# Kernel optimization log

Hardware: AMD Instinct MI355X
Metric: run time of the kernel (lower is better)

## Reference

```python
import jax, jax.numpy as jnp
import numpy as np

N_EMBD = 1024
N_HEAD = 16
HEAD_DIM = N_EMBD // N_HEAD


def setup_inputs() -> dict:
    key = jax.random.key(0)
    kx, kq, kk, kv, ko = jax.random.split(key, 5)
    B, T = 4, 2048
    x = jax.random.normal(kx, (B, T, N_EMBD), dtype=jnp.float32)
    s = N_EMBD ** -0.5
    Wq = jax.random.normal(kq, (N_EMBD, N_EMBD), dtype=jnp.float32) * s
    Wk = jax.random.normal(kk, (N_EMBD, HEAD_DIM), dtype=jnp.float32) * s
    Wv = jax.random.normal(kv, (N_EMBD, HEAD_DIM), dtype=jnp.float32) * s
    Wo = jax.random.normal(ko, (N_EMBD, N_EMBD), dtype=jnp.float32) * s
    return {"x": x, "Wq": Wq, "Wk": Wk, "Wv": Wv, "Wo": Wo}


def reference(x, Wq, Wk, Wv, Wo):
    B, T, C = x.shape
    scale = HEAD_DIM ** -0.5
    # q: [B, H, T, D]; shared k, v: [B, T, D]
    q = (x @ Wq).reshape(B, T, N_HEAD, HEAD_DIM).transpose(0, 2, 1, 3)
    k = x @ Wk
    v = x @ Wv
    # scores: [B, H, T, T] (shared K head broadcast over H)
    att = jnp.einsum('bhtd,bsd->bhts', q, k) * scale
    causal = jnp.tril(jnp.ones((T, T), dtype=bool))
    att = jnp.where(causal, att, -jnp.inf)
    att = jax.nn.softmax(att, axis=-1)
    out = jnp.einsum('bhts,bsd->bhtd', att, v)  # [B, H, T, D]
    out = out.transpose(0, 2, 1, 3).reshape(B, T, C)
    return out @ Wo
```

## Files before the change

### kernel.cpp

```cpp
#include <hip/hip_runtime.h>

typedef __attribute__((ext_vector_type(8))) short short8;
typedef __attribute__((ext_vector_type(4))) float f32x4;

__device__ __forceinline__ unsigned short f2bf(float f) {
  unsigned u = __builtin_bit_cast(unsigned, f);
  u += 0x7fffu + ((u >> 16) & 1u);
  return (unsigned short)(u >> 16);
}
__device__ __forceinline__ unsigned pack_bf2_rtz(float p0, float p1) {
  return __builtin_amdgcn_perm(__builtin_bit_cast(unsigned, p1),
                               __builtin_bit_cast(unsigned, p0), 0x07060302u);
}

#define GLDS16(g, l)                                                          \
  __builtin_amdgcn_global_load_lds(                                           \
      (const __attribute__((address_space(1))) void*)(g),                     \
      (__attribute__((address_space(3))) void*)(l), 16, 0, 0)

#define QSCALE 0.18033688011112042f

__global__ void cast_x_bf16(const float4* __restrict__ in,
                            ushort4* __restrict__ out, int n4) {
  int i = blockIdx.x * blockDim.x + threadIdx.x;
  if (i >= n4) return;
  float4 v = in[i];
  ushort4 o;
  o.x = f2bf(v.x); o.y = f2bf(v.y); o.z = f2bf(v.z); o.w = f2bf(v.w);
  out[i] = o;
}

__global__ void transpose_cvt_all(const float* __restrict__ Wq,
                                  const float* __restrict__ Wk,
                                  const float* __restrict__ Wv,
                                  const float* __restrict__ Wo,
                                  unsigned short* __restrict__ Wcat,
                                  unsigned short* __restrict__ Wot) {
  __shared__ float tile[32][33];
  const int z = blockIdx.z;
  int bx = blockIdx.x;
  const float* in;
  unsigned short* out;
  int N;
  if (z == 0)      { in = Wq; out = Wcat;               N = 1024; }
  else if (z == 1) { in = Wo; out = Wot;                N = 1024; }
  else {
    if (bx < 2)      { in = Wk; out = Wcat + 1024 * 1024; N = 64; }
    else if (bx < 4) { in = Wv; out = Wcat + 1088 * 1024; N = 64; bx -= 2; }
    else return;
  }
  const int K = 1024;
  const int n0 = bx * 32, k0 = blockIdx.y * 32;
  const int tx = threadIdx.x, ty = threadIdx.y;
#pragma unroll
  for (int i = 0; i < 4; ++i)
    tile[ty + 8 * i][tx] = in[(size_t)(k0 + ty + 8 * i) * N + n0 + tx];
  __syncthreads();
#pragma unroll
  for (int i = 0; i < 4; ++i)
    out[(size_t)(n0 + ty + 8 * i) * K + k0 + tx] = f2bf(tile[tx][ty + 8 * i]);
}

__global__ void transpose_v(const unsigned short* __restrict__ Vr,
                            unsigned short* __restrict__ Vt) {
  __shared__ unsigned short tile[32][34];
  const int t0 = blockIdx.x * 32;
  const int d0 = blockIdx.y * 32;
  const int b = blockIdx.z;
  const int tx = threadIdx.x, ty = threadIdx.y;
#pragma unroll
  for (int i = 0; i < 4; ++i)
    tile[ty + 8 * i][tx] =
        Vr[(size_t)(b * 2048 + t0 + ty + 8 * i) * 64 + d0 + tx];
  __syncthreads();
#pragma unroll
  for (int i = 0; i < 4; ++i)
    Vt[((size_t)b * 64 + d0 + ty + 8 * i) * 2048 + t0 + tx] =
        tile[tx][ty + 8 * i];
}

template <int EPI>
__global__ __launch_bounds__(256) void gemm_bt(
    const unsigned short* __restrict__ A, const unsigned short* __restrict__ Bt,
    unsigned short* __restrict__ Cq, unsigned short* __restrict__ Ck,
    unsigned short* __restrict__ Cv, float* __restrict__ Cf, int N, int K) {
  __shared__ __align__(16) unsigned short As[128 * 64];
  __shared__ __align__(16) unsigned short Bs[128 * 64];
  const int tid = threadIdx.x;
  const int w = tid >> 6, lane = tid & 63;
  const int nwg = gridDim.x * gridDim.y;
  const int lid = blockIdx.y * gridDim.x + blockIdx.x;
  const int cpx = nwg >> 3;
  const int swz = (lid & 7) * cpx + (lid >> 3);
  const int m0 = (swz / gridDim.x) * 128, n0 = (swz % gridDim.x) * 128;
  const int wm = (w >> 1) * 64, wn = (w & 1) * 64;
  const int g = lane >> 4, c = lane & 15;
  const int lr = lane >> 3, lc = (lane & 7) * 8;

  f32x4 acc[4][4] = {};

  for (int k0 = 0; k0 < K; k0 += 64) {
#pragma unroll
    for (int i = 0; i < 4; ++i) {
      int ci = w * 4 + i;
      GLDS16(A + (size_t)(m0 + ci * 8 + lr) * K + k0 + lc, As + ci * 512);
      GLDS16(Bt + (size_t)(n0 + ci * 8 + lr) * K + k0 + lc, Bs + ci * 512);
    }
    __syncthreads();
#pragma unroll
    for (int kk = 0; kk < 2; ++kk) {
      const int col = kk * 32 + g * 8;
      short8 av[4], bv[4];
#pragma unroll
      for (int mi = 0; mi < 4; ++mi)
        av[mi] = *(const short8*)(As + (wm + mi * 16 + c) * 64 + col);
#pragma unroll
      for (int ni = 0; ni < 4; ++ni)
        bv[ni] = *(const short8*)(Bs + (wn + ni * 16 + c) * 64 + col);
#pragma unroll
      for (int mi = 0; mi < 4; ++mi)
#pragma unroll
        for (int ni = 0; ni < 4; ++ni)
          acc[mi][ni] = __builtin_amdgcn_mfma_f32_16x16x32_bf16(
              av[mi], bv[ni], acc[mi][ni], 0, 0, 0);
    }
    __syncthreads();
  }

#pragma unroll
  for (int mi = 0; mi < 4; ++mi) {
#pragma unroll
    for (int ni = 0; ni < 4; ++ni) {
      f32x4 a = acc[mi][ni];
      const int col = n0 + wn + ni * 16 + c;
#pragma unroll
      for (int r = 0; r < 4; ++r) {
        const int row = m0 + wm + mi * 16 + g * 4 + r;
        float v = a[r];
        if (EPI == 0) {
          if (col < 1024)
            Cq[(size_t)row * 1024 + col] = f2bf(v * QSCALE);
          else if (col < 1088)
            Ck[(size_t)row * 64 + (col - 1024)] = f2bf(v);
          else
            Cv[(size_t)row * 64 + (col - 1088)] = f2bf(v);
        } else {
          Cf[(size_t)row * N + col] = v;
        }
      }
    }
  }
}

__global__ __launch_bounds__(256, 3) void attn_mqa(
    const unsigned short* __restrict__ Q, const unsigned short* __restrict__ Kb,
    const unsigned short* __restrict__ Vt, unsigned short* __restrict__ Oc) {
  __shared__ __align__(16) unsigned short Kl[2][64 * 64];
  __shared__ __align__(16) unsigned short Vl[2][64 * 64];
  __shared__ __align__(16) unsigned short Pl[4][32 * 72];
  const int tid = threadIdx.x;
  const int w = tid >> 6, lane = tid & 63;
  const int bid = blockIdx.x;
  const int b = bid & 3;
  const int h = (bid >> 2) & 15;
  const int qidx = (bid >> 6) & 15;
  const int qt = 15 - qidx;
  const int g = lane >> 4, c = lane & 15;
  const int swr = (c & 7) * 8;
  const int srow8 = tid >> 3;
  const int scs = ((tid & 7) ^ (srow8 & 7)) * 8;
  const unsigned short* Kbase = Kb + (size_t)b * 2048 * 64;
  const unsigned short* Vbase = Vt + (size_t)b * 64 * 2048;
  unsigned short* pw = Pl[w];
  unsigned* pd = (unsigned*)pw;

  short8 ones;
#pragma unroll
  for (int j = 0; j < 8; ++j) ones[j] = (short)0x3F80;

  const int qb = qt * 128 + w * 32;

  short8 qf[2][2];
#pragma unroll
  for (int u = 0; u < 2; ++u)
#pragma unroll
    for (int kk = 0; kk < 2; ++kk)
      qf[u][kk] = *(const short8*)(Q + (size_t)(b * 2048 + qb + u * 16 + c) *
                                           1024 + h * 64 + kk * 32 + g * 8);

  f32x4 po[2][4] = {};
  f32x4 lac[2] = {};
  float m[2] = {-1e30f, -1e30f};

  const unsigned short* kpf = Kbase + (size_t)srow8 * 64 + scs;
  const unsigned short* vpf = Vbase + (size_t)srow8 * 2048 + scs;
  GLDS16(kpf, &Kl[0][0] + tid * 8);
  GLDS16(kpf + 2048, &Kl[0][0] + tid * 8 + 2048);
  GLDS16(vpf, &Vl[0][0] + tid * 8);
  GLDS16(vpf + 65536, &Vl[0][0] + tid * 8 + 2048);
  kpf += 4096;
  vpf += 64;
  int cur = 0;
  const int nit = 2 * qt + 2;

  for (int it = 0; it < nit; ++it) {
    __syncthreads();

    if (it < nit - 1) {
      unsigned short* kd = &Kl[cur ^ 1][0] + tid * 8;
      unsigned short* vd = &Vl[cur ^ 1][0] + tid * 8;
      GLDS16(kpf, kd);
      GLDS16(kpf + 2048, kd + 2048);
      GLDS16(vpf, vd);
      GLDS16(vpf + 65536, vd + 2048);
      kpf += 4096;
      vpf += 64;
    }

    const unsigned short* Kt = &Kl[cur][0];
    const unsigned short* Vc = &Vl[cur][0];
    const int kv0 = it * 64;

    f32x4 s[2][4] = {};
    __builtin_amdgcn_s_setprio(1);
#pragma unroll
    for (int kk = 0; kk < 2; ++kk) {
      const int col = (kk * 32 + g * 8) ^ swr;
#pragma unroll
      for (int f = 0; f < 4; ++f) {
        short8 kf = *(const short8*)(Kt + (f * 16 + c) * 64 + col);
        s[0][f] = __builtin_amdgcn_mfma_f32_16x16x32_bf16(kf, qf[0][kk],
                                                          s[0][f], 0, 0, 0);
        s[1][f] = __builtin_amdgcn_mfma_f32_16x16x32_bf16(kf, qf[1][kk],
                                                          s[1][f], 0, 0, 0);
      }
    }
    __builtin_amdgcn_s_setprio(0);

    float pm[2];
#pragma unroll
    for (int u = 0; u < 2; ++u) {
      if (kv0 + 63 > qb + u * 16) {
        const int qi = qb + u * 16 + c;
#pragma unroll
        for (int f = 0; f < 4; ++f)
#pragma unroll
          for (int r = 0; r < 4; ++r)
            if (kv0 + f * 16 + g * 4 + r > qi) s[u][f][r] = -1e30f;
      }
      const float t0 = fmaxf(fmaxf(s[u][0][0], s[u][0][1]), s[u][0][2]);
      const float t1 = fmaxf(fmaxf(s[u][0][3], s[u][1][0]), s[u][1][1]);
      const float t2 = fmaxf(fmaxf(s[u][1][2], s[u][1][3]), s[u][2][0]);
      const float t3 = fmaxf(fmaxf(s[u][2][1], s[u][2][2]), s[u][2][3]);
      const float t4 = fmaxf(fmaxf(s[u][3][0], s[u][3][1]), s[u][3][2]);
      const float u0 = fmaxf(fmaxf(t0, t1), t2);
      const float u1 = fmaxf(fmaxf(t3, t4), s[u][3][3]);
      pm[u] = fmaxf(u0, u1);
    }

    if (!__all(pm[0] <= m[0] + 8.0f && pm[1] <= m[1] + 8.0f)) {
#pragma unroll
      for (int u = 0; u < 2; ++u) {
        float pmu = fmaxf(pm[u], __shfl_xor(pm[u], 16, 64));
        pmu = fmaxf(pmu, __shfl_xor(pmu, 32, 64));
        const float mn = fmaxf(m[u], pmu);
        const float al = __builtin_amdgcn_exp2f(m[u] - mn);
        m[u] = mn;
#pragma unroll
        for (int r = 0; r < 4; ++r) {
          const float ar = __shfl(al, g * 4 + r, 64);
          lac[u][r] *= ar;
#pragma unroll
          for (int fd = 0; fd < 4; ++fd) po[u][fd][r] *= ar;
        }
      }
    }

#pragma unroll
    for (int u = 0; u < 2; ++u) {
#pragma unroll
      for (int f = 0; f < 4; ++f) {
        const float p0 = __builtin_amdgcn_exp2f(s[u][f][0] - m[u]);
        const float p1 = __builtin_amdgcn_exp2f(s[u][f][1] - m[u]);
        const float p2 = __builtin_amdgcn_exp2f(s[u][f][2] - m[u]);
        const float p3 = __builtin_amdgcn_exp2f(s[u][f][3] - m[u]);
        uint2 pk;
        pk.x = pack_bf2_rtz(p0, p1);
        pk.y = pack_bf2_rtz(p2, p3);
        *(uint2*)(pd + (u * 16 + c) * 36 + f * 8 + g * 2) = pk;
      }
    }

    __builtin_amdgcn_s_setprio(1);
#pragma unroll
    for (int kk = 0; kk < 2; ++kk) {
      short8 pa0 = *(const short8*)(pw + c * 72 + kk * 32 + g * 8);
      short8 pa1 = *(const short8*)(pw + (16 + c) * 72 + kk * 32 + g * 8);
      lac[0] = __builtin_amdgcn_mfma_f32_16x16x32_bf16(pa0, ones, lac[0], 0, 0, 0);
      lac[1] = __builtin_amdgcn_mfma_f32_16x16x32_bf16(pa1, ones, lac[1], 0, 0, 0);
      const int col = (kk * 32 + g * 8) ^ swr;
#pragma unroll
      for (int fd = 0; fd < 4; ++fd) {
        short8 vf = *(const short8*)(Vc + (fd * 16 + c) * 64 + col);
        po[0][fd] = __builtin_amdgcn_mfma_f32_16x16x32_bf16(pa0, vf, po[0][fd],
                                                            0, 0, 0);
        po[1][fd] = __builtin_amdgcn_mfma_f32_16x16x32_bf16(pa1, vf, po[1][fd],
                                                            0, 0, 0);
      }
    }
    __builtin_amdgcn_s_setprio(0);
    cur ^= 1;
  }

#pragma unroll
  for (int u = 0; u < 2; ++u) {
#pragma unroll
    for (int r = 0; r < 4; ++r) {
      const float inv = __builtin_amdgcn_rcpf(lac[u][r]);
      const int trow = qb + u * 16 + g * 4 + r;
#pragma unroll
      for (int fd = 0; fd < 4; ++fd)
        Oc[(size_t)(b * 2048 + trow) * 1024 + h * 64 + fd * 16 + c] =
            f2bf(po[u][fd][r] * inv);
    }
  }
}

extern "C" void kernel_launch(void* const* d_in, const int* in_sizes, int n_in,
                              void* d_out, int out_size, void* d_ws,
                              size_t ws_size, hipStream_t stream) {
  const float* x = (const float*)d_in[0];
  const float* Wq = (const float*)d_in[1];
  const float* Wk = (const float*)d_in[2];
  const float* Wv = (const float*)d_in[3];
  const float* Wo = (const float*)d_in[4];
  float* out = (float*)d_out;

  char* ws = (char*)d_ws;
  unsigned short* xb   = (unsigned short*)ws;
  unsigned short* Qb   = (unsigned short*)(ws + (size_t)(16u << 20));
  unsigned short* Attn = (unsigned short*)(ws + (size_t)(32u << 20));
  unsigned short* Wcat = (unsigned short*)(ws + (size_t)(48u << 20));
  unsigned short* Wot  = (unsigned short*)(ws + (size_t)(48u << 20) + 2359296);
  unsigned short* Kb   = (unsigned short*)(ws + (size_t)(48u << 20) + 2359296 + 2097152);
  unsigned short* Vtb  = (unsigned short*)(ws + (size_t)(48u << 20) + 2359296 + 2097152 + 1048576);
  unsigned short* Vrow = Attn;

  cast_x_bf16<<<8192, 256, 0, stream>>>((const float4*)x, (ushort4*)xb, 2097152);
  transpose_cvt_all<<<dim3(32, 32, 3), dim3(32, 8), 0, stream>>>(Wq, Wk, Wv, Wo,
                                                                 Wcat, Wot);

  gemm_bt<0><<<dim3(9, 64), 256, 0, stream>>>(xb, Wcat, Qb, Kb, Vrow, nullptr,
                                              1152, 1024);
  transpose_v<<<dim3(64, 2, 4), dim3(32, 8), 0, stream>>>(Vrow, Vtb);

  attn_mqa<<<1024, 256, 0, stream>>>(Qb, Kb, Vtb, Attn);

  gemm_bt<1><<<dim3(8, 64), 256, 0, stream>>>(Attn, Wot, nullptr, nullptr,
                                              nullptr, out, 1024, 1024);
}
```

Measured before the change: 146.9 us.

## Load K/V fragments directly from global memory, dropping LDS staging and barriers

The attention kernel no longer stages K and V tiles through double-buffered shared memory with async global-to-LDS copies and per-iteration __syncthreads. Each wave now reads its MFMA K and V fragments straight from global memory (through the cache), and the launch bound is raised from 3 to 4 blocks per SM now that LDS use has shrunk. This removes the barrier and LDS traffic, and since K/V are shared across heads they should be cache-resident. In exchange, global-load latency lands directly in the compute loop with no prefetch, and each of the four waves fetches the same K/V data redundantly.

```diff
diff --git a/kernel.cpp b/kernel.cpp
--- a/kernel.cpp
+++ b/kernel.cpp
@@ -152,11 +152,9 @@
   }
 }
 
-__global__ __launch_bounds__(256, 3) void attn_mqa(
+__global__ __launch_bounds__(256, 4) void attn_mqa(
     const unsigned short* __restrict__ Q, const unsigned short* __restrict__ Kb,
     const unsigned short* __restrict__ Vt, unsigned short* __restrict__ Oc) {
-  __shared__ __align__(16) unsigned short Kl[2][64 * 64];
-  __shared__ __align__(16) unsigned short Vl[2][64 * 64];
   __shared__ __align__(16) unsigned short Pl[4][32 * 72];
   const int tid = threadIdx.x;
   const int w = tid >> 6, lane = tid & 63;
@@ -166,9 +164,6 @@
   const int qidx = (bid >> 6) & 15;
   const int qt = 15 - qidx;
   const int g = lane >> 4, c = lane & 15;
-  const int swr = (c & 7) * 8;
-  const int srow8 = tid >> 3;
-  const int scs = ((tid & 7) ^ (srow8 & 7)) * 8;
   const unsigned short* Kbase = Kb + (size_t)b * 2048 * 64;
   const unsigned short* Vbase = Vt + (size_t)b * 64 * 2048;
   unsigned short* pw = Pl[w];
@@ -192,43 +187,18 @@
   f32x4 lac[2] = {};
   float m[2] = {-1e30f, -1e30f};
 
-  const unsigned short* kpf = Kbase + (size_t)srow8 * 64 + scs;
-  const unsigned short* vpf = Vbase + (size_t)srow8 * 2048 + scs;
-  GLDS16(kpf, &Kl[0][0] + tid * 8);
-  GLDS16(kpf + 2048, &Kl[0][0] + tid * 8 + 2048);
-  GLDS16(vpf, &Vl[0][0] + tid * 8);
-  GLDS16(vpf + 65536, &Vl[0][0] + tid * 8 + 2048);
-  kpf += 4096;
-  vpf += 64;
-  int cur = 0;
+  const unsigned short* kfp = Kbase + (size_t)c * 64 + g * 8;
+  const unsigned short* vfp = Vbase + (size_t)c * 2048 + g * 8;
   const int nit = 2 * qt + 2;
 
   for (int it = 0; it < nit; ++it) {
-    __syncthreads();
-
-    if (it < nit - 1) {
-      unsigned short* kd = &Kl[cur ^ 1][0] + tid * 8;
-      unsigned short* vd = &Vl[cur ^ 1][0] + tid * 8;
-      GLDS16(kpf, kd);
-      GLDS16(kpf + 2048, kd + 2048);
-      GLDS16(vpf, vd);
-      GLDS16(vpf + 65536, vd + 2048);
-      kpf += 4096;
-      vpf += 64;
-    }
-
-    const unsigned short* Kt = &Kl[cur][0];
-    const unsigned short* Vc = &Vl[cur][0];
-    const int kv0 = it * 64;
-
     f32x4 s[2][4] = {};
     __builtin_amdgcn_s_setprio(1);
 #pragma unroll
     for (int kk = 0; kk < 2; ++kk) {
-      const int col = (kk * 32 + g * 8) ^ swr;
 #pragma unroll
       for (int f = 0; f < 4; ++f) {
-        short8 kf = *(const short8*)(Kt + (f * 16 + c) * 64 + col);
+        short8 kf = *(const short8*)(kfp + (size_t)f * 1024 + kk * 32);
         s[0][f] = __builtin_amdgcn_mfma_f32_16x16x32_bf16(kf, qf[0][kk],
                                                           s[0][f], 0, 0, 0);
         s[1][f] = __builtin_amdgcn_mfma_f32_16x16x32_bf16(kf, qf[1][kk],
@@ -237,6 +207,7 @@
     }
     __builtin_amdgcn_s_setprio(0);
 
+    const int kv0 = it * 64;
     float pm[2];
 #pragma unroll
     for (int u = 0; u < 2; ++u) {
@@ -298,10 +269,9 @@
       short8 pa1 = *(const short8*)(pw + (16 + c) * 72 + kk * 32 + g * 8);
       lac[0] = __builtin_amdgcn_mfma_f32_16x16x32_bf16(pa0, ones, lac[0], 0, 0, 0);
       lac[1] = __builtin_amdgcn_mfma_f32_16x16x32_bf16(pa1, ones, lac[1], 0, 0, 0);
-      const int col = (kk * 32 + g * 8) ^ swr;
 #pragma unroll
       for (int fd = 0; fd < 4; ++fd) {
-        short8 vf = *(const short8*)(Vc + (fd * 16 + c) * 64 + col);
+        short8 vf = *(const short8*)(vfp + (size_t)fd * 32768 + kk * 32);
         po[0][fd] = __builtin_amdgcn_mfma_f32_16x16x32_bf16(pa0, vf, po[0][fd],
                                                             0, 0, 0);
         po[1][fd] = __builtin_amdgcn_mfma_f32_16x16x32_bf16(pa1, vf, po[1][fd],
@@ -309,7 +279,9 @@
       }
     }
     __builtin_amdgcn_s_setprio(0);
-    cur ^= 1;
+
+    kfp += 64 * 64;
+    vfp += 64;
   }
 
 #pragma unroll
```

After: 254.0 us, median of 4. 73.0% more time.
